# Optimization experiments

Hardware: AMD Instinct MI355X
Metric: run time of the kernel (lower is better)

The kernel has to match this reference:

```python
import jax, jax.numpy as jnp
import numpy as np

N_NODES = 50000
N_EDGES = 800000
IN_DIM = 128
HID = 128
N_GRAPHS = 256
N_CLASSES = 2
ALPHA = 0.2  # leaky relu slope
EPS_BN = 1e-5


def setup_inputs() -> dict:
    key = jax.random.key(0)
    ks = jax.random.split(key, 24)
    adjacency = jax.random.randint(ks[0], (2, N_EDGES), 0, N_NODES, dtype=jnp.int32)
    input_feature = jax.random.normal(ks[1], (N_NODES, IN_DIM), dtype=jnp.float32)
    graph_indicator = jnp.sort(jax.random.randint(ks[2], (N_NODES,), 0, N_GRAPHS, dtype=jnp.int32))
    labels = jax.random.randint(ks[3], (N_GRAPHS,), 0, N_CLASSES, dtype=jnp.int64)
    s = 0.05
    params = {
        'W1': jax.random.normal(ks[4], (IN_DIM, HID), jnp.float32) * s,
        'a1': jax.random.normal(ks[5], (2 * HID,), jnp.float32) * s,
        'bn2_g': jnp.ones((HID,), jnp.float32),
        'bn2_b': jnp.zeros((HID,), jnp.float32),
        'W2': jax.random.normal(ks[6], (HID, HID), jnp.float32) * s,
        'a2': jax.random.normal(ks[7], (2 * HID,), jnp.float32) * s,
        'bn3_g': jnp.ones((HID,), jnp.float32),
        'bn3_b': jnp.zeros((HID,), jnp.float32),
        'W3': jax.random.normal(ks[8], (HID, HID), jnp.float32) * s,
        'a3': jax.random.normal(ks[9], (2 * HID,), jnp.float32) * s,
        'fc1_w': jax.random.normal(ks[10], (HID, 2 * HID), jnp.float32) * s,
        'fc1_b': jnp.zeros((2 * HID,), jnp.float32),
        'fc2_w': jax.random.normal(ks[11], (2 * HID, HID), jnp.float32) * s,
        'fc2_b': jnp.zeros((HID,), jnp.float32),
        'fc3_w': jax.random.normal(ks[12], (HID, N_CLASSES), jnp.float32) * s,
        'fc3_b': jnp.zeros((N_CLASSES,), jnp.float32),
    }
    return dict(adjacency=adjacency, input_feature=input_feature,
                graph_indicator=graph_indicator, labels=labels, **params)


def _batchnorm(x, g, b):
    # training-mode BatchNorm1d over node dim (biased variance)
    mu = jnp.mean(x, axis=0)
    var = jnp.mean((x - mu) ** 2, axis=0)
    return (x - mu) * jax.lax.rsqrt(var + EPS_BN) * g + b


def _sp_gat(x, src, dst, W, a):
    # pyGAT SpGraphAttentionLayer (dropout disabled / eval mode)
    h = x @ W                                # [N, F]
    F = h.shape[1]
    e_src = h @ a[:F]                        # [N]
    e_dst = h @ a[F:]                        # [N]
    e = e_src[src] + e_dst[dst]              # [E]
    ee = jnp.exp(-jax.nn.leaky_relu(e, ALPHA))
    rowsum = jax.ops.segment_sum(ee, src, num_segments=N_NODES)          # [N]
    num = jax.ops.segment_sum(ee[:, None] * h[dst], src, num_segments=N_NODES)  # [N, F]
    h_prime = num / (rowsum[:, None] + 1e-16)
    return jax.nn.elu(h_prime)


def reference(adjacency, input_feature, graph_indicator, labels,
              W1, a1, bn2_g, bn2_b, W2, a2, bn3_g, bn3_b, W3, a3,
              fc1_w, fc1_b, fc2_w, fc2_b, fc3_w, fc3_b):
    src, dst = adjacency[0], adjacency[1]
    # bn1 output is discarded in the original forward
    x = _sp_gat(input_feature, src, dst, W1, a1)
    x = _batchnorm(x, bn2_g, bn2_b)
    x = _sp_gat(x, src, dst, W2, a2)
    x = _batchnorm(x, bn3_g, bn3_b)
    x = _sp_gat(x, src, dst, W3, a3)
    # pooling_sum_4tensor: per-graph sum pooling
    pooled = jax.ops.segment_sum(x, graph_indicator, num_segments=N_GRAPHS)  # [G, F]
    x = jax.nn.relu(pooled @ fc1_w + fc1_b)
    x = jax.nn.relu(x @ fc2_w + fc2_b)
    logits = x @ fc3_w + fc3_b
    return logits
```

## Files before the change

### kernel.cpp

```cpp
#include <hip/hip_runtime.h>
#include <hip/hip_bf16.h>

#define N_NODES 50000
#define N_EDGES 800000
#define FD 128
#define N_GRAPHS 256
#define NPART 6250

typedef unsigned short u16;
typedef short bf16x8 __attribute__((ext_vector_type(8)));
typedef float f32x4 __attribute__((ext_vector_type(4)));

__device__ __forceinline__ u16 f2bf(float v) {
    __hip_bfloat16 h = __float2bfloat16(v);
    union { __hip_bfloat16 hh; u16 u; } c; c.hh = h; return c.u;
}
__device__ __forceinline__ float bf2f(u16 r) {
    return __uint_as_float(((unsigned int)r) << 16);
}

__global__ __launch_bounds__(256) void count_deg_part_k(const int* __restrict__ src,
                                                        int* __restrict__ cnt, int E) {
    int part = blockIdx.x & 7;
    int lo = part * NPART, hi = lo + NPART;
    int stride = (gridDim.x >> 3) * 256;
    for (int e = (blockIdx.x >> 3) * 256 + threadIdx.x; e < E; e += stride) {
        int s = src[e];
        if (s >= lo && s < hi) atomicAdd(&cnt[s], 1);
    }
}

__global__ __launch_bounds__(256) void fill_csr_part_k(const int* __restrict__ src,
                                                       const int* __restrict__ dst,
                                                       int* __restrict__ cur,
                                                       int* __restrict__ edst, int E) {
    int part = blockIdx.x & 7;
    int lo = part * NPART, hi = lo + NPART;
    int stride = (gridDim.x >> 3) * 256;
    for (int e = (blockIdx.x >> 3) * 256 + threadIdx.x; e < E; e += stride) {
        int s = src[e];
        if (s >= lo && s < hi) {
            int p = atomicAdd(&cur[s], 1);
            edst[p] = dst[e];
        }
    }
}

__global__ __launch_bounds__(256) void scan1_k(const int* __restrict__ cnt,
                                               int* __restrict__ bsum, int M) {
    int i = blockIdx.x * 256 + threadIdx.x;
    int v = (i < M) ? cnt[i] : 0;
    __shared__ int l[256];
    l[threadIdx.x] = v;
    __syncthreads();
    for (int s = 128; s > 0; s >>= 1) {
        if (threadIdx.x < s) l[threadIdx.x] += l[threadIdx.x + s];
        __syncthreads();
    }
    if (threadIdx.x == 0) bsum[blockIdx.x] = l[0];
}

__global__ __launch_bounds__(256) void scan2_k(int* __restrict__ bsum, int NB) {
    int tid = threadIdx.x;
    int v = (tid < NB) ? bsum[tid] : 0;
    __shared__ int l[256];
    l[tid] = v;
    __syncthreads();
    for (int off = 1; off < 256; off <<= 1) {
        int t = (tid >= off) ? l[tid - off] : 0;
        __syncthreads();
        l[tid] += t;
        __syncthreads();
    }
    if (tid < NB) bsum[tid] = l[tid] - v;
}

__global__ __launch_bounds__(256) void scan3_k(const int* __restrict__ cnt,
                                               const int* __restrict__ bsum,
                                               int* __restrict__ offs,
                                               int* __restrict__ cur, int M) {
    int i = blockIdx.x * 256 + threadIdx.x;
    int tid = threadIdx.x;
    int v = (i < M) ? cnt[i] : 0;
    __shared__ int l[256];
    l[tid] = v;
    __syncthreads();
    for (int off = 1; off < 256; off <<= 1) {
        int t = (tid >= off) ? l[tid - off] : 0;
        __syncthreads();
        l[tid] += t;
        __syncthreads();
    }
    int excl = l[tid] - v + bsum[blockIdx.x];
    if (i < M) { offs[i] = excl; cur[i] = excl; }
    if (i == M - 1) offs[M] = excl + v;
}

__global__ __launch_bounds__(256) void cvt_in_k(const float* __restrict__ X,
                                                u16* __restrict__ Xb, int n4) {
    int i = blockIdx.x * 256 + threadIdx.x;
    if (i < n4) {
        float4 v = ((const float4*)X)[i];
        ushort4 o;
        o.x = f2bf(v.x); o.y = f2bf(v.y); o.z = f2bf(v.z); o.w = f2bf(v.w);
        ((ushort4*)Xb)[i] = o;
    }
}

__global__ __launch_bounds__(128) void wprep_k(const float* __restrict__ W,
                                               const float* __restrict__ scale,
                                               const float* __restrict__ shift,
                                               u16* __restrict__ Wt,
                                               float* __restrict__ cvec) {
    int n = blockIdx.x, k = threadIdx.x;
    float w = W[(size_t)k * FD + n];
    Wt[(size_t)n * FD + k] = f2bf(scale[k] * w);
    __shared__ float l[128];
    l[k] = shift[k] * w;
    __syncthreads();
    for (int s = 64; s > 0; s >>= 1) {
        if (k < s) l[k] += l[k + s];
        __syncthreads();
    }
    if (k == 0) cvec[n] = l[0];
}

__global__ __launch_bounds__(256) void gemm_mfma_k(const u16* __restrict__ Xb,
                                                   const u16* __restrict__ Wt,
                                                   const float* __restrict__ cvec,
                                                   const float* __restrict__ avec,
                                                   u16* __restrict__ Hb,
                                                   float* __restrict__ es,
                                                   float* __restrict__ ed, int M) {
    __shared__ u16 As[64][136];
    __shared__ u16 Bs[128][136];
    __shared__ float sa_s[128], sa_d[128], cv[128];
    int tid = threadIdx.x;
    if (tid < 128) { sa_s[tid] = avec[tid]; sa_d[tid] = avec[128 + tid]; cv[tid] = cvec[tid]; }
    int row0 = blockIdx.x * 64;
    {
        int n = tid >> 1, k0 = (tid & 1) * 64;
        const uint4* s = (const uint4*)(Wt + (size_t)n * FD + k0);
#pragma unroll
        for (int u = 0; u < 8; u++) *(uint4*)&Bs[n][k0 + u * 8] = s[u];
    }
    {
        int r = tid >> 2, k0 = (tid & 3) * 32;
        int grow = row0 + r;
        if (grow < M) {
            const uint4* s = (const uint4*)(Xb + (size_t)grow * FD + k0);
#pragma unroll
            for (int u = 0; u < 4; u++) *(uint4*)&As[r][k0 + u * 8] = s[u];
        } else {
            uint4 z = make_uint4(0, 0, 0, 0);
#pragma unroll
            for (int u = 0; u < 4; u++) *(uint4*)&As[r][k0 + u * 8] = z;
        }
    }
    __syncthreads();

    int wave = tid >> 6, lane = tid & 63;
    int quad = lane >> 4, n16 = lane & 15;
    int rbase = wave * 16;
    f32x4 acc[8];
    f32x4 zz = {0.f, 0.f, 0.f, 0.f};
#pragma unroll
    for (int t = 0; t < 8; t++) acc[t] = zz;

#pragma unroll
    for (int kk = 0; kk < 128; kk += 32) {
        bf16x8 a = *(const bf16x8*)&As[rbase + n16][kk + quad * 8];
#pragma unroll
        for (int t = 0; t < 8; t++) {
            bf16x8 b = *(const bf16x8*)&Bs[t * 16 + n16][kk + quad * 8];
            acc[t] = __builtin_amdgcn_mfma_f32_16x16x32_bf16(a, b, acc[t], 0, 0, 0);
        }
    }

#pragma unroll
    for (int reg = 0; reg < 4; reg++) {
        int grow = row0 + rbase + quad * 4 + reg;
        float vals[8];
        float ps = 0.f, pd = 0.f;
#pragma unroll
        for (int t = 0; t < 8; t++) {
            float v = acc[t][reg] + cv[t * 16 + n16];
            vals[t] = v;
            ps += v * sa_s[t * 16 + n16];
            pd += v * sa_d[t * 16 + n16];
        }
#pragma unroll
        for (int o = 8; o > 0; o >>= 1) { ps += __shfl_xor(ps, o); pd += __shfl_xor(pd, o); }
        if (grow < M) {
            if (n16 == 0) { es[grow] = ps; ed[grow] = pd; }
#pragma unroll
            for (int t = 0; t < 8; t++)
                Hb[(size_t)grow * FD + t * 16 + n16] = f2bf(vals[t]);
        }
    }
}

__global__ __launch_bounds__(256) void agg_k(const u16* __restrict__ Hb,
                                             const float* __restrict__ es_,
                                             const float* __restrict__ ed_,
                                             const int* __restrict__ offs,
                                             const int* __restrict__ edst,
                                             u16* __restrict__ OutB,
                                             float* __restrict__ OutF,
                                             int fp32out, int M) {
    int node = __builtin_amdgcn_readfirstlane((int)((blockIdx.x * blockDim.x + threadIdx.x) >> 6));
    int lane = threadIdx.x & 63;
    if (node >= M) return;
    int s0 = offs[node], s1 = offs[node + 1];
    float esv = es_[node];
    const unsigned int* Hrow = (const unsigned int*)Hb;
    float2 a0 = make_float2(0.f, 0.f), a1 = make_float2(0.f, 0.f);
    float2 a2 = make_float2(0.f, 0.f), a3 = make_float2(0.f, 0.f);
    float rs = 0.f;
    int e = s0;
    for (; e + 8 <= s1; e += 8) {
        int d[8];
#pragma unroll
        for (int u = 0; u < 8; u++) d[u] = __builtin_amdgcn_readfirstlane(edst[e + u]);
        float w[8];
#pragma unroll
        for (int u = 0; u < 8; u++) {
            float ev = esv + ed_[d[u]];
            float lr = ev > 0.f ? ev : 0.2f * ev;
            w[u] = __expf(-lr);
        }
        unsigned int r[8];
#pragma unroll
        for (int u = 0; u < 8; u++) r[u] = Hrow[(size_t)d[u] * 64 + lane];
#pragma unroll
        for (int u = 0; u < 8; u++) {
            rs += w[u];
            float2* ac = (u & 3) == 0 ? &a0 : (u & 3) == 1 ? &a1 : (u & 3) == 2 ? &a2 : &a3;
            ac->x += w[u] * __int_as_float(r[u] << 16);
            ac->y += w[u] * __int_as_float(r[u] & 0xffff0000u);
        }
    }
    for (; e < s1; e++) {
        int d = __builtin_amdgcn_readfirstlane(edst[e]);
        float ev = esv + ed_[d];
        float lr = ev > 0.f ? ev : 0.2f * ev;
        float wv = __expf(-lr);
        rs += wv;
        unsigned int r = Hrow[(size_t)d * 64 + lane];
        a0.x += wv * __int_as_float(r << 16);
        a0.y += wv * __int_as_float(r & 0xffff0000u);
    }
    float inv = 1.f / (rs + 1e-16f);
    float vx = (a0.x + a1.x + a2.x + a3.x) * inv;
    float vy = (a0.y + a1.y + a2.y + a3.y) * inv;
    vx = vx > 0.f ? vx : (__expf(vx) - 1.f);
    vy = vy > 0.f ? vy : (__expf(vy) - 1.f);
    if (fp32out) {
        ((float2*)OutF)[(size_t)node * 64 + lane] = make_float2(vx, vy);
    } else {
        unsigned int pk = ((unsigned int)f2bf(vy) << 16) | f2bf(vx);
        ((unsigned int*)OutB)[(size_t)node * 64 + lane] = pk;
    }
}

__global__ void bnstats_b_k(const u16* __restrict__ Xb, float* __restrict__ sums,
                            float* __restrict__ sumsq, int M) {
    int f = threadIdx.x & 127;
    int half = threadIdx.x >> 7;
    float s1 = 0.f, s2 = 0.f;
    for (int r = blockIdx.x * 2 + half; r < M; r += gridDim.x * 2) {
        float v = bf2f(Xb[(size_t)r * FD + f]);
        s1 += v; s2 += v * v;
    }
    __shared__ float l1[256], l2[256];
    l1[threadIdx.x] = s1; l2[threadIdx.x] = s2;
    __syncthreads();
    if (half == 0) {
        atomicAdd(&sums[f], l1[f] + l1[f + 128]);
        atomicAdd(&sumsq[f], l2[f] + l2[f + 128]);
    }
}

__global__ void init_affine_k(float* scale, float* shift, float* sums, float* sumsq) {
    int f = threadIdx.x;
    scale[f] = 1.f; shift[f] = 0.f; sums[f] = 0.f; sumsq[f] = 0.f;
}

__global__ void bnfinal_k(float* sums, float* sumsq, const float* __restrict__ g,
                          const float* __restrict__ b, float* scale, float* shift, float invN) {
    int f = threadIdx.x;
    float mu = sums[f] * invN;
    float var = sumsq[f] * invN - mu * mu;
    float sc = g[f] * rsqrtf(var + 1e-5f);
    scale[f] = sc;
    shift[f] = b[f] - mu * sc;
    sums[f] = 0.f; sumsq[f] = 0.f;
}

__global__ void pool_k(const float* __restrict__ X, const int* __restrict__ gi,
                       float* __restrict__ pooled, int M) {
    int f = threadIdx.x & 127;
    int half = threadIdx.x >> 7;
    int r0 = blockIdx.x * 128 + half;
    int rend = min(blockIdx.x * 128 + 128, M);
    int curg = -1; float acc = 0.f;
    for (int r = r0; r < rend; r += 2) {
        int g = gi[r];
        if (g != curg) {
            if (curg >= 0) atomicAdd(&pooled[(size_t)curg * FD + f], acc);
            curg = g; acc = 0.f;
        }
        acc += X[(size_t)r * FD + f];
    }
    if (curg >= 0) atomicAdd(&pooled[(size_t)curg * FD + f], acc);
}

__global__ void fc_relu_k(const float* __restrict__ X, const float* __restrict__ Wt,
                          const float* __restrict__ b, float* __restrict__ Y,
                          int K, int Ncols) {
    int g = blockIdx.x;
    int j = threadIdx.x;
    extern __shared__ float xrow[];
    for (int k = threadIdx.x; k < K; k += blockDim.x) xrow[k] = X[(size_t)g * K + k];
    __syncthreads();
    float s = b[j];
    for (int k = 0; k < K; k++) s += xrow[k] * Wt[(size_t)k * Ncols + j];
    Y[(size_t)g * Ncols + j] = fmaxf(s, 0.f);
}

__global__ void fc3_k(const float* __restrict__ X, const float* __restrict__ W,
                      const float* __restrict__ b, float* __restrict__ out) {
    int g = blockIdx.x;
    int l = threadIdx.x;
    float2 x2 = ((const float2*)X)[g * 64 + l];
    float s0 = x2.x * W[(2 * l) * 2]     + x2.y * W[(2 * l + 1) * 2];
    float s1 = x2.x * W[(2 * l) * 2 + 1] + x2.y * W[(2 * l + 1) * 2 + 1];
#pragma unroll
    for (int o = 32; o > 0; o >>= 1) { s0 += __shfl_xor(s0, o); s1 += __shfl_xor(s1, o); }
    if (l == 0) { out[g * 2] = s0 + b[0]; out[g * 2 + 1] = s1 + b[1]; }
}

extern "C" void kernel_launch(void* const* d_in, const int* in_sizes, int n_in,
                              void* d_out, int out_size, void* d_ws, size_t ws_size,
                              hipStream_t stream) {
    const int*   adj  = (const int*)d_in[0];
    const float* xin  = (const float*)d_in[1];
    const int*   gi   = (const int*)d_in[2];
    const float* W1   = (const float*)d_in[4];
    const float* a1   = (const float*)d_in[5];
    const float* bn2g = (const float*)d_in[6];
    const float* bn2b = (const float*)d_in[7];
    const float* W2   = (const float*)d_in[8];
    const float* a2   = (const float*)d_in[9];
    const float* bn3g = (const float*)d_in[10];
    const float* bn3b = (const float*)d_in[11];
    const float* W3   = (const float*)d_in[12];
    const float* a3   = (const float*)d_in[13];
    const float* fc1w = (const float*)d_in[14];
    const float* fc1b = (const float*)d_in[15];
    const float* fc2w = (const float*)d_in[16];
    const float* fc2b = (const float*)d_in[17];
    const float* fc3w = (const float*)d_in[18];
    const float* fc3b = (const float*)d_in[19];
    float* out = (float*)d_out;

    const int N = N_NODES, E = N_EDGES, G = N_GRAPHS;

    float* buf1   = (float*)d_ws;
    u16*   Xb     = (u16*)(buf1 + (size_t)N * FD);
    u16*   Hb     = Xb + (size_t)N * FD;
    u16*   Wt     = Hb + (size_t)N * FD;
    float* es     = (float*)(Wt + FD * FD);
    float* ed     = es + N;
    float* scale  = ed + N;
    float* shift  = scale + FD;
    float* sums   = shift + FD;
    float* sumsq  = sums + FD;
    float* cvec   = sumsq + FD;
    float* pooled = cvec + FD;
    float* t1     = pooled + (size_t)G * FD;
    float* t2     = t1 + (size_t)G * 256;
    int*   degcnt = (int*)(t2 + (size_t)G * FD);
    int*   offs   = degcnt + N;
    int*   cur    = offs + (N + 2);
    int*   bsum   = cur + N;
    int*   edst   = bsum + 256;

    const int* srcp = adj;
    const int* dstp = adj + E;

    const int NB = (N + 255) / 256;

    hipMemsetAsync(degcnt, 0, (size_t)N * sizeof(int), stream);
    count_deg_part_k<<<8 * 392, 256, 0, stream>>>(srcp, degcnt, E);
    scan1_k<<<NB, 256, 0, stream>>>(degcnt, bsum, N);
    scan2_k<<<1, 256, 0, stream>>>(bsum, NB);
    scan3_k<<<NB, 256, 0, stream>>>(degcnt, bsum, offs, cur, N);
    fill_csr_part_k<<<8 * 392, 256, 0, stream>>>(srcp, dstp, cur, edst, E);
    init_affine_k<<<1, 128, 0, stream>>>(scale, shift, sums, sumsq);
    cvt_in_k<<<(N * FD / 4 + 255) / 256, 256, 0, stream>>>(xin, Xb, N * FD / 4);

    const int gemm_grid = (N + 63) / 64;
    const int wave_grid = (N + 3) / 4;
    const float invN = 1.0f / (float)N;

    wprep_k<<<FD, 128, 0, stream>>>(W1, scale, shift, Wt, cvec);
    gemm_mfma_k<<<gemm_grid, 256, 0, stream>>>(Xb, Wt, cvec, a1, Hb, es, ed, N);
    agg_k<<<wave_grid, 256, 0, stream>>>(Hb, es, ed, offs, edst, Xb, buf1, 0, N);
    bnstats_b_k<<<256, 256, 0, stream>>>(Xb, sums, sumsq, N);
    bnfinal_k<<<1, 128, 0, stream>>>(sums, sumsq, bn2g, bn2b, scale, shift, invN);

    wprep_k<<<FD, 128, 0, stream>>>(W2, scale, shift, Wt, cvec);
    gemm_mfma_k<<<gemm_grid, 256, 0, stream>>>(Xb, Wt, cvec, a2, Hb, es, ed, N);
    agg_k<<<wave_grid, 256, 0, stream>>>(Hb, es, ed, offs, edst, Xb, buf1, 0, N);
    bnstats_b_k<<<256, 256, 0, stream>>>(Xb, sums, sumsq, N);
    bnfinal_k<<<1, 128, 0, stream>>>(sums, sumsq, bn3g, bn3b, scale, shift, invN);

    wprep_k<<<FD, 128, 0, stream>>>(W3, scale, shift, Wt, cvec);
    gemm_mfma_k<<<gemm_grid, 256, 0, stream>>>(Xb, Wt, cvec, a3, Hb, es, ed, N);
    agg_k<<<wave_grid, 256, 0, stream>>>(Hb, es, ed, offs, edst, Xb, buf1, 1, N);

    hipMemsetAsync(pooled, 0, (size_t)G * FD * sizeof(float), stream);
    pool_k<<<(N + 127) / 128, 256, 0, stream>>>(buf1, gi, pooled, N);
    fc_relu_k<<<G, 256, FD * sizeof(float), stream>>>(pooled, fc1w, fc1b, t1, FD, 256);
    fc_relu_k<<<G, 128, 256 * sizeof(float), stream>>>(t1, fc2w, fc2b, t2, 256, FD);
    fc3_k<<<G, 64, 0, stream>>>(t2, fc3w, fc3b, out);
}
```

Measured before the change: 459.3 us.

## Fuse input conversion, BN finalize and MLP stages to cut kernel launches

Folds the fp32->bf16 input conversion into the first GEMM's tile load and merges the BN finalize step into the weight-prep kernel. Zeroing of the BN accumulators moves into scan2, and the three FC kernels become one MLP kernel. The last aggregation now writes bf16 instead of fp32, so pooling reads the smaller buffer. This removes several small launches and one full pass over the input, at the cost of slightly lower precision in the pooled sum.

Result: faster. 432.6 us (-5.8%).

```diff
diff --git a/kernel.cpp b/kernel.cpp
--- a/kernel.cpp
+++ b/kernel.cpp
@@ -60,8 +60,10 @@
     if (threadIdx.x == 0) bsum[blockIdx.x] = l[0];
 }
 
-__global__ __launch_bounds__(256) void scan2_k(int* __restrict__ bsum, int NB) {
+__global__ __launch_bounds__(256) void scan2_k(int* __restrict__ bsum, int NB,
+                                               float* __restrict__ z) {
     int tid = threadIdx.x;
+    z[tid] = 0.f; z[tid + 256] = 0.f;
     int v = (tid < NB) ? bsum[tid] : 0;
     __shared__ int l[256];
     l[tid] = v;
@@ -96,27 +98,33 @@
     if (i == M - 1) offs[M] = excl + v;
 }
 
-__global__ __launch_bounds__(256) void cvt_in_k(const float* __restrict__ X,
-                                                u16* __restrict__ Xb, int n4) {
-    int i = blockIdx.x * 256 + threadIdx.x;
-    if (i < n4) {
-        float4 v = ((const float4*)X)[i];
-        ushort4 o;
-        o.x = f2bf(v.x); o.y = f2bf(v.y); o.z = f2bf(v.z); o.w = f2bf(v.w);
-        ((ushort4*)Xb)[i] = o;
-    }
-}
-
-__global__ __launch_bounds__(128) void wprep_k(const float* __restrict__ W,
-                                               const float* __restrict__ scale,
-                                               const float* __restrict__ shift,
-                                               u16* __restrict__ Wt,
-                                               float* __restrict__ cvec) {
+__global__ __launch_bounds__(128) void wprep1_k(const float* __restrict__ W,
+                                                u16* __restrict__ Wt,
+                                                float* __restrict__ cvec) {
     int n = blockIdx.x, k = threadIdx.x;
+    Wt[(size_t)n * FD + k] = f2bf(W[(size_t)k * FD + n]);
+    if (k == 0) cvec[n] = 0.f;
+}
+
+__global__ __launch_bounds__(128) void bnfw_k(const float* __restrict__ W,
+                                              const float* __restrict__ sums,
+                                              const float* __restrict__ sumsq,
+                                              const float* __restrict__ g,
+                                              const float* __restrict__ b,
+                                              float invN,
+                                              u16* __restrict__ Wt,
+                                              float* __restrict__ cvec) {
+    int n = blockIdx.x, k = threadIdx.x;
+    __shared__ float scs[128], shs[128], l[128];
+    float mu = sums[k] * invN;
+    float var = sumsq[k] * invN - mu * mu;
+    float sc = g[k] * rsqrtf(var + 1e-5f);
+    scs[k] = sc;
+    shs[k] = b[k] - mu * sc;
+    __syncthreads();
     float w = W[(size_t)k * FD + n];
-    Wt[(size_t)n * FD + k] = f2bf(scale[k] * w);
-    __shared__ float l[128];
-    l[k] = shift[k] * w;
+    Wt[(size_t)n * FD + k] = f2bf(scs[k] * w);
+    l[k] = shs[k] * w;
     __syncthreads();
     for (int s = 64; s > 0; s >>= 1) {
         if (k < s) l[k] += l[k + s];
@@ -125,7 +133,9 @@
     if (k == 0) cvec[n] = l[0];
 }
 
-__global__ __launch_bounds__(256) void gemm_mfma_k(const u16* __restrict__ Xb,
+__global__ __launch_bounds__(256) void gemm_mfma_k(const float* __restrict__ Xf,
+                                                   const u16* __restrict__ Xb,
+                                                   int use_f32,
                                                    const u16* __restrict__ Wt,
                                                    const float* __restrict__ cvec,
                                                    const float* __restrict__ avec,
@@ -148,9 +158,20 @@
         int r = tid >> 2, k0 = (tid & 3) * 32;
         int grow = row0 + r;
         if (grow < M) {
-            const uint4* s = (const uint4*)(Xb + (size_t)grow * FD + k0);
-#pragma unroll
-            for (int u = 0; u < 4; u++) *(uint4*)&As[r][k0 + u * 8] = s[u];
+            if (use_f32) {
+                const float4* s = (const float4*)(Xf + (size_t)grow * FD + k0);
+#pragma unroll
+                for (int u = 0; u < 8; u++) {
+                    float4 v = s[u];
+                    ushort4 o;
+                    o.x = f2bf(v.x); o.y = f2bf(v.y); o.z = f2bf(v.z); o.w = f2bf(v.w);
+                    *(ushort4*)&As[r][k0 + u * 4] = o;
+                }
+            } else {
+                const uint4* s = (const uint4*)(Xb + (size_t)grow * FD + k0);
+#pragma unroll
+                for (int u = 0; u < 4; u++) *(uint4*)&As[r][k0 + u * 8] = s[u];
+            }
         } else {
             uint4 z = make_uint4(0, 0, 0, 0);
 #pragma unroll
@@ -205,9 +226,7 @@
                                              const float* __restrict__ ed_,
                                              const int* __restrict__ offs,
                                              const int* __restrict__ edst,
-                                             u16* __restrict__ OutB,
-                                             float* __restrict__ OutF,
-                                             int fp32out, int M) {
+                                             u16* __restrict__ Out, int M) {
     int node = __builtin_amdgcn_readfirstlane((int)((blockIdx.x * blockDim.x + threadIdx.x) >> 6));
     int lane = threadIdx.x & 63;
     if (node >= M) return;
@@ -255,12 +274,8 @@
     float vy = (a0.y + a1.y + a2.y + a3.y) * inv;
     vx = vx > 0.f ? vx : (__expf(vx) - 1.f);
     vy = vy > 0.f ? vy : (__expf(vy) - 1.f);
-    if (fp32out) {
-        ((float2*)OutF)[(size_t)node * 64 + lane] = make_float2(vx, vy);
-    } else {
-        unsigned int pk = ((unsigned int)f2bf(vy) << 16) | f2bf(vx);
-        ((unsigned int*)OutB)[(size_t)node * 64 + lane] = pk;
-    }
+    unsigned int pk = ((unsigned int)f2bf(vy) << 16) | f2bf(vx);
+    ((unsigned int*)Out)[(size_t)node * 64 + lane] = pk;
 }
 
 __global__ void bnstats_b_k(const u16* __restrict__ Xb, float* __restrict__ sums,
@@ -281,23 +296,7 @@
     }
 }
 
-__global__ void init_affine_k(float* scale, float* shift, float* sums, float* sumsq) {
-    int f = threadIdx.x;
-    scale[f] = 1.f; shift[f] = 0.f; sums[f] = 0.f; sumsq[f] = 0.f;
-}
-
-__global__ void bnfinal_k(float* sums, float* sumsq, const float* __restrict__ g,
-                          const float* __restrict__ b, float* scale, float* shift, float invN) {
-    int f = threadIdx.x;
-    float mu = sums[f] * invN;
-    float var = sumsq[f] * invN - mu * mu;
-    float sc = g[f] * rsqrtf(var + 1e-5f);
-    scale[f] = sc;
-    shift[f] = b[f] - mu * sc;
-    sums[f] = 0.f; sumsq[f] = 0.f;
-}
-
-__global__ void pool_k(const float* __restrict__ X, const int* __restrict__ gi,
+__global__ void pool_k(const u16* __restrict__ Xb, const int* __restrict__ gi,
                        float* __restrict__ pooled, int M) {
     int f = threadIdx.x & 127;
     int half = threadIdx.x >> 7;
@@ -310,34 +309,37 @@
             if (curg >= 0) atomicAdd(&pooled[(size_t)curg * FD + f], acc);
             curg = g; acc = 0.f;
         }
-        acc += X[(size_t)r * FD + f];
+        acc += bf2f(Xb[(size_t)r * FD + f]);
     }
     if (curg >= 0) atomicAdd(&pooled[(size_t)curg * FD + f], acc);
 }
 
-__global__ void fc_relu_k(const float* __restrict__ X, const float* __restrict__ Wt,
-                          const float* __restrict__ b, float* __restrict__ Y,
-                          int K, int Ncols) {
-    int g = blockIdx.x;
-    int j = threadIdx.x;
-    extern __shared__ float xrow[];
-    for (int k = threadIdx.x; k < K; k += blockDim.x) xrow[k] = X[(size_t)g * K + k];
-    __syncthreads();
-    float s = b[j];
-    for (int k = 0; k < K; k++) s += xrow[k] * Wt[(size_t)k * Ncols + j];
-    Y[(size_t)g * Ncols + j] = fmaxf(s, 0.f);
-}
-
-__global__ void fc3_k(const float* __restrict__ X, const float* __restrict__ W,
-                      const float* __restrict__ b, float* __restrict__ out) {
-    int g = blockIdx.x;
-    int l = threadIdx.x;
-    float2 x2 = ((const float2*)X)[g * 64 + l];
-    float s0 = x2.x * W[(2 * l) * 2]     + x2.y * W[(2 * l + 1) * 2];
-    float s1 = x2.x * W[(2 * l) * 2 + 1] + x2.y * W[(2 * l + 1) * 2 + 1];
-#pragma unroll
-    for (int o = 32; o > 0; o >>= 1) { s0 += __shfl_xor(s0, o); s1 += __shfl_xor(s1, o); }
-    if (l == 0) { out[g * 2] = s0 + b[0]; out[g * 2 + 1] = s1 + b[1]; }
+__global__ __launch_bounds__(256) void mlp_k(const float* __restrict__ pooled,
+                                             const float* __restrict__ fc1w, const float* __restrict__ fc1b,
+                                             const float* __restrict__ fc2w, const float* __restrict__ fc2b,
+                                             const float* __restrict__ fc3w, const float* __restrict__ fc3b,
+                                             float* __restrict__ out) {
+    int g = blockIdx.x, j = threadIdx.x;
+    __shared__ float x[128], t1[256], t2[128], p0[128], p1[128];
+    if (j < 128) x[j] = pooled[(size_t)g * FD + j];
+    __syncthreads();
+    float s = fc1b[j];
+    for (int k = 0; k < 128; k++) s += x[k] * fc1w[(size_t)k * 256 + j];
+    t1[j] = fmaxf(s, 0.f);
+    __syncthreads();
+    if (j < 128) {
+        float s2 = fc2b[j];
+        for (int k = 0; k < 256; k++) s2 += t1[k] * fc2w[(size_t)k * 128 + j];
+        t2[j] = fmaxf(s2, 0.f);
+    }
+    __syncthreads();
+    if (j < 128) { p0[j] = t2[j] * fc3w[j * 2]; p1[j] = t2[j] * fc3w[j * 2 + 1]; }
+    __syncthreads();
+    for (int s3 = 64; s3 > 0; s3 >>= 1) {
+        if (j < s3) { p0[j] += p0[j + s3]; p1[j] += p1[j + s3]; }
+        __syncthreads();
+    }
+    if (j == 0) { out[g * 2] = p0[0] + fc3b[0]; out[g * 2 + 1] = p1[0] + fc3b[1]; }
 }
 
 extern "C" void kernel_launch(void* const* d_in, const int* in_sizes, int n_in,
@@ -366,21 +368,19 @@
 
     const int N = N_NODES, E = N_EDGES, G = N_GRAPHS;
 
-    float* buf1   = (float*)d_ws;
-    u16*   Xb     = (u16*)(buf1 + (size_t)N * FD);
+    u16*   Xb     = (u16*)d_ws;
     u16*   Hb     = Xb + (size_t)N * FD;
     u16*   Wt     = Hb + (size_t)N * FD;
     float* es     = (float*)(Wt + FD * FD);
     float* ed     = es + N;
-    float* scale  = ed + N;
-    float* shift  = scale + FD;
-    float* sums   = shift + FD;
-    float* sumsq  = sums + FD;
-    float* cvec   = sumsq + FD;
+    float* bnbuf  = ed + N;
+    float* sumsA  = bnbuf;
+    float* sumsqA = bnbuf + 128;
+    float* sumsB  = bnbuf + 256;
+    float* sumsqB = bnbuf + 384;
+    float* cvec   = bnbuf + 512;
     float* pooled = cvec + FD;
-    float* t1     = pooled + (size_t)G * FD;
-    float* t2     = t1 + (size_t)G * 256;
-    int*   degcnt = (int*)(t2 + (size_t)G * FD);
+    int*   degcnt = (int*)(pooled + (size_t)G * FD);
     int*   offs   = degcnt + N;
     int*   cur    = offs + (N + 2);
     int*   bsum   = cur + N;
@@ -394,35 +394,29 @@
     hipMemsetAsync(degcnt, 0, (size_t)N * sizeof(int), stream);
     count_deg_part_k<<<8 * 392, 256, 0, stream>>>(srcp, degcnt, E);
     scan1_k<<<NB, 256, 0, stream>>>(degcnt, bsum, N);
-    scan2_k<<<1, 256, 0, stream>>>(bsum, NB);
+    scan2_k<<<1, 256, 0, stream>>>(bsum, NB, bnbuf);
     scan3_k<<<NB, 256, 0, stream>>>(degcnt, bsum, offs, cur, N);
     fill_csr_part_k<<<8 * 392, 256, 0, stream>>>(srcp, dstp, cur, edst, E);
-    init_affine_k<<<1, 128, 0, stream>>>(scale, shift, sums, sumsq);
-    cvt_in_k<<<(N * FD / 4 + 255) / 256, 256, 0, stream>>>(xin, Xb, N * FD / 4);
 
     const int gemm_grid = (N + 63) / 64;
     const int wave_grid = (N + 3) / 4;
     const float invN = 1.0f / (float)N;
 
-    wprep_k<<<FD, 128, 0, stream>>>(W1, scale, shift, Wt, cvec);
-    gemm_mfma_k<<<gemm_grid, 256, 0, stream>>>(Xb, Wt, cvec, a1, Hb, es, ed, N);
-    agg_k<<<wave_grid, 256, 0, stream>>>(Hb, es, ed, offs, edst, Xb, buf1, 0, N);
-    bnstats_b_k<<<256, 256, 0, stream>>>(Xb, sums, sumsq, N);
-    bnfinal_k<<<1, 128, 0, stream>>>(sums, sumsq, bn2g, bn2b, scale, shift, invN);
-
-    wprep_k<<<FD, 128, 0, stream>>>(W2, scale, shift, Wt, cvec);
-    gemm_mfma_k<<<gemm_grid, 256, 0, stream>>>(Xb, Wt, cvec, a2, Hb, es, ed, N);
-    agg_k<<<wave_grid, 256, 0, stream>>>(Hb, es, ed, offs, edst, Xb, buf1, 0, N);
-    bnstats_b_k<<<256, 256, 0, stream>>>(Xb, sums, sumsq, N);
-    bnfinal_k<<<1, 128, 0, stream>>>(sums, sumsq, bn3g, bn3b, scale, shift, invN);
-
-    wprep_k<<<FD, 128, 0, stream>>>(W3, scale, shift, Wt, cvec);
-    gemm_mfma_k<<<gemm_grid, 256, 0, stream>>>(Xb, Wt, cvec, a3, Hb, es, ed, N);
-    agg_k<<<wave_grid, 256, 0, stream>>>(Hb, es, ed, offs, edst, Xb, buf1, 1, N);
+    wprep1_k<<<FD, 128, 0, stream>>>(W1, Wt, cvec);
+    gemm_mfma_k<<<gemm_grid, 256, 0, stream>>>(xin, Xb, 1, Wt, cvec, a1, Hb, es, ed, N);
+    agg_k<<<wave_grid, 256, 0, stream>>>(Hb, es, ed, offs, edst, Xb, N);
+    bnstats_b_k<<<256, 256, 0, stream>>>(Xb, sumsA, sumsqA, N);
+
+    bnfw_k<<<FD, 128, 0, stream>>>(W2, sumsA, sumsqA, bn2g, bn2b, invN, Wt, cvec);
+    gemm_mfma_k<<<gemm_grid, 256, 0, stream>>>(nullptr, Xb, 0, Wt, cvec, a2, Hb, es, ed, N);
+    agg_k<<<wave_grid, 256, 0, stream>>>(Hb, es, ed, offs, edst, Xb, N);
+    bnstats_b_k<<<256, 256, 0, stream>>>(Xb, sumsB, sumsqB, N);
+
+    bnfw_k<<<FD, 128, 0, stream>>>(W3, sumsB, sumsqB, bn3g, bn3b, invN, Wt, cvec);
+    gemm_mfma_k<<<gemm_grid, 256, 0, stream>>>(nullptr, Xb, 0, Wt, cvec, a3, Hb, es, ed, N);
+    agg_k<<<wave_grid, 256, 0, stream>>>(Hb, es, ed, offs, edst, Xb, N);
 
     hipMemsetAsync(pooled, 0, (size_t)G * FD * sizeof(float), stream);
-    pool_k<<<(N + 127) / 128, 256, 0, stream>>>(buf1, gi, pooled, N);
-    fc_relu_k<<<G, 256, FD * sizeof(float), stream>>>(pooled, fc1w, fc1b, t1, FD, 256);
-    fc_relu_k<<<G, 128, 256 * sizeof(float), stream>>>(t1, fc2w, fc2b, t2, 256, FD);
-    fc3_k<<<G, 64, 0, stream>>>(t2, fc3w, fc3b, out);
-}
+    pool_k<<<(N + 127) / 128, 256, 0, stream>>>(Xb, gi, pooled, N);
+    mlp_k<<<G, 256, 0, stream>>>(pooled, fc1w, fc1b, fc2w, fc2b, fc3w, fc3b, out);
+}
```
